# Kernel tuning notes

Hardware: AMD Instinct MI355X
Metric: run time of the kernel (lower is better)

The kernel has to match this reference:

```python
import jax, jax.numpy as jnp
import numpy as np

D_IN, D_HID = 64, 128

def _ff(x, w1, b1, w2, b2):
    # FeedForward: Linear -> ReLU -> Linear
    return jax.nn.relu(x @ w1 + b1) @ w2 + b2

def setup_inputs() -> dict:
    key = jax.random.key(0)
    ks = jax.random.split(key, 10)
    N, m = 8, 2048
    def lin(k, fan_in, fan_out):
        bound = 1.0 / np.sqrt(fan_in)
        return jax.random.uniform(k, (fan_in, fan_out), jnp.float32, -bound, bound)
    return {
        "x": jax.random.normal(ks[0], (N, m, D_IN), jnp.float32),
        "edge": jax.random.uniform(ks[1], (N, m, m), jnp.float32),
        # f: dim_in -> dim_hid//2 -> dim_hid
        "f_w1": lin(ks[2], D_IN, D_HID // 2),
        "f_b1": jnp.zeros((D_HID // 2,), jnp.float32),
        "f_w2": lin(ks[3], D_HID // 2, D_HID),
        "f_b2": jnp.zeros((D_HID,), jnp.float32),
        # g: 2*dim_in -> dim_hid -> dim_hid
        "g_w1": lin(ks[4], 2 * D_IN, D_HID),
        "g_b1": jnp.zeros((D_HID,), jnp.float32),
        "g_w2": lin(ks[5], D_HID, D_HID),
        "g_b2": jnp.zeros((D_HID,), jnp.float32),
    }

def reference(x, edge, f_w1, f_b1, f_w2, f_b2, g_w1, g_b1, g_w2, g_b2):
    # self dynamics: f(x) -> [N, m, D_HID]
    self_dyn = _ff(x, f_w1, f_b1, f_w2, f_b2)
    # Original builds interaction[n,i,j] = cat(x[n,i], x[n,i]) (receiver is
    # transposed twice), so g is constant along j. Compute g once per sender node.
    gx = _ff(jnp.concatenate([x, x], axis=-1), g_w1, g_b1, g_w2, g_b2)  # [N, m, H]
    # interaction.sum over sender dim i with edge weights: out[n,j] = sum_i edge[n,i,j]*gx[n,i]
    inter = jnp.einsum('nij,nih->njh', edge, gx)
    return self_dyn + inter
```

## Files before the change

kernel.cpp:

```cpp
#include <hip/hip_runtime.h>


typedef __attribute__((ext_vector_type(8))) short bf16x8;
typedef __attribute__((ext_vector_type(8))) unsigned short u16x8;
typedef __attribute__((ext_vector_type(4))) unsigned short u16x4;
typedef __attribute__((ext_vector_type(4))) float f32x4;
typedef __attribute__((ext_vector_type(8))) float f32x8;

static __device__ __forceinline__ unsigned short f2bf(float f) {
  union { float f; unsigned int i; } c; c.f = f;
  return (unsigned short)((c.i + 0x7fffu + ((c.i >> 16) & 1u)) >> 16);
}

__global__ __launch_bounds__(256) void k_gx(
    const float* __restrict__ x,
    const float* __restrict__ gw1,
    const float* __restrict__ gb1,
    const float* __restrict__ gw2,
    const float* __restrict__ gb2,
    unsigned short* __restrict__ gxT)
{
  __shared__ short xs[64 * 64];
  __shared__ short w1T[128 * 64];
  __shared__ short w2T[128 * 128];
  __shared__ short h2s[64 * 128];

  const int t = threadIdx.x;
  const int R0 = blockIdx.x * 64;

  for (int idx = t; idx < 64 * 128; idx += 256) {
    int k = idx >> 7, n = idx & 127;
    float v = gw1[idx] + gw1[64 * 128 + idx];
    w1T[(n << 6) + (((k >> 3) ^ (n & 7)) << 3) + (k & 7)] = (short)f2bf(v);
  }
  for (int idx = t; idx < 128 * 128; idx += 256) {
    int k = idx >> 7, n = idx & 127;
    w2T[(n << 7) + (((k >> 3) ^ (n & 7)) << 3) + (k & 7)] = (short)f2bf(gw2[idx]);
  }
  for (int s = t; s < 64 * 16; s += 256) {
    int row = s >> 4, c4 = s & 15;
    f32x4 v = *(const f32x4*)(x + (size_t)(R0 + row) * 64 + c4 * 4);
    u16x4 pk;
#pragma unroll
    for (int r = 0; r < 4; ++r) pk[r] = f2bf(v[r]);
    *(u16x4*)(xs + (row << 6) + (((c4 >> 1) ^ (row & 7)) << 3) + ((c4 & 1) << 2)) = pk;
  }
  __syncthreads();

  const int w = t >> 6, l = t & 63;
  const int lr = l & 15, q = l >> 4;
  const int mrow = w * 16 + lr;

  bf16x8 a[2];
#pragma unroll
  for (int ks = 0; ks < 2; ++ks) {
    int c = ks * 4 + q;
    a[ks] = *(const bf16x8*)(xs + (mrow << 6) + ((c ^ (mrow & 7)) << 3));
  }

  f32x4 acc;
#pragma unroll
  for (int nf = 0; nf < 8; ++nf) {
    acc = (f32x4){0.f, 0.f, 0.f, 0.f};
#pragma unroll
    for (int ks = 0; ks < 2; ++ks) {
      int c = ks * 4 + q;
      int nr = nf * 16 + lr;
      bf16x8 b = *(const bf16x8*)(w1T + (nr << 6) + ((c ^ (nr & 7)) << 3));
      acc = __builtin_amdgcn_mfma_f32_16x16x32_bf16(a[ks], b, acc, 0, 0, 0);
    }
    float bias = gb1[nf * 16 + lr];
#pragma unroll
    for (int r = 0; r < 4; ++r) {
      float v = acc[r] + bias;
      v = v > 0.f ? v : 0.f;
      int row = w * 16 + q * 4 + r, n = nf * 16 + lr;
      h2s[(row << 7) + (((n >> 3) ^ (row & 7)) << 3) + (n & 7)] = (short)f2bf(v);
    }
  }
  __syncthreads();

  bf16x8 a2[4];
#pragma unroll
  for (int ks = 0; ks < 4; ++ks) {
    int c = ks * 4 + q;
    a2[ks] = *(const bf16x8*)(h2s + (mrow << 7) + ((c ^ (mrow & 7)) << 3));
  }
  const int batch = R0 >> 11;
  const int ib = R0 & 2047;
#pragma unroll
  for (int nf = 0; nf < 8; ++nf) {
    acc = (f32x4){0.f, 0.f, 0.f, 0.f};
#pragma unroll
    for (int ks = 0; ks < 4; ++ks) {
      int c = ks * 4 + q;
      int nr = nf * 16 + lr;
      bf16x8 b = *(const bf16x8*)(w2T + (nr << 7) + ((c ^ (nr & 7)) << 3));
      acc = __builtin_amdgcn_mfma_f32_16x16x32_bf16(a2[ks], b, acc, 0, 0, 0);
    }
    float bias = gb2[nf * 16 + lr];
    u16x4 pk;
#pragma unroll
    for (int r = 0; r < 4; ++r) pk[r] = f2bf(acc[r] + bias);
    *(u16x4*)(gxT + (size_t)(batch * 128 + nf * 16 + lr) * 2048 + ib + w * 16 + q * 4) = pk;
  }
}

__device__ __forceinline__ void load_tiles(const float* ep, const unsigned short* gp,
                                           f32x8& er, u16x8 gr[4])
{
  er = *(const f32x8*)ep;
#pragma unroll
  for (int qq = 0; qq < 4; ++qq)
    gr[qq] = *(const u16x8*)(gp + (size_t)qq * 32 * 2048);
}

__global__ __launch_bounds__(256) void k_main(
    const float* __restrict__ edge,
    const unsigned short* __restrict__ gxT,
    const float* __restrict__ x,
    const float* __restrict__ fw1,
    const float* __restrict__ fb1,
    const float* __restrict__ fw2,
    const float* __restrict__ fb2,
    float* __restrict__ out)
{
  __shared__ short eT[32 * 72];
  __shared__ short bT[128 * 64];
  __shared__ short xs[32 * 64];
  __shared__ short w1T[64 * 64];
  __shared__ short h1s[32 * 64];

  const int t = threadIdx.x;
  const int batch = blockIdx.x & 7;
  const int j0 = (blockIdx.x >> 3) * 32;

  const int w = t >> 6, l = t & 63;
  const int wm = w & 1, wn = w >> 1;
  const int lr = l & 15, q = l >> 4;

  const int e_ii = t >> 2;
  const int e_cj = t & 3;
  const int g_hh = t >> 3;
  const int g_ci = t & 7;

  const float* ep = edge + (size_t)batch * 2048 * 2048 + (size_t)e_ii * 2048 + j0 + e_cj * 8;
  const unsigned short* gp = gxT + (size_t)batch * 128 * 2048 + (size_t)g_hh * 2048 + g_ci * 8;

  f32x4 acc[4];
#pragma unroll
  for (int nf = 0; nf < 4; ++nf) acc[nf] = (f32x4){0.f, 0.f, 0.f, 0.f};

  f32x8 er;
  u16x8 gr[4];
  load_tiles(ep, gp, er, gr);

  for (int kk = 0; kk < 32; ++kk) {
    __syncthreads();
#pragma unroll
    for (int u = 0; u < 8; ++u)
      eT[(e_cj * 8 + u) * 72 + (((e_ii >> 3) ^ e_cj) << 3) + (e_ii & 7)] = (short)f2bf(er[u]);
#pragma unroll
    for (int qq = 0; qq < 4; ++qq) {
      int r = qq * 32 + g_hh;
      *(u16x8*)(bT + (r << 6) + ((g_ci ^ (r & 7)) << 3)) = gr[qq];
    }
    __syncthreads();
    if (kk < 31) {
      ep += 64 * 2048; gp += 64;
      load_tiles(ep, gp, er, gr);
    }

#pragma unroll
    for (int ks = 0; ks < 2; ++ks) {
      const int c = ks * 4 + q;
      const int jj = wm * 16 + lr;
      bf16x8 a = *(const bf16x8*)(eT + jj * 72 + ((c ^ (jj >> 3)) << 3));
      bf16x8 b[4];
#pragma unroll
      for (int nf = 0; nf < 4; ++nf) {
        int h = wn * 64 + nf * 16 + lr;
        b[nf] = *(const bf16x8*)(bT + (h << 6) + ((c ^ (h & 7)) << 3));
      }
#pragma unroll
      for (int nf = 0; nf < 4; ++nf)
        acc[nf] = __builtin_amdgcn_mfma_f32_16x16x32_bf16(a, b[nf], acc[nf], 0, 0, 0);
    }
  }

  __syncthreads();
  for (int idx = t; idx < 64 * 64; idx += 256) {
    int k = idx >> 6, n = idx & 63;
    w1T[(n << 6) + (((k >> 3) ^ (n & 7)) << 3) + (k & 7)] = (short)f2bf(fw1[idx]);
  }
  for (int idx = t; idx < 64 * 128; idx += 256) {
    int k = idx >> 7, n = idx & 127;
    bT[(n << 6) + (((k >> 3) ^ (n & 7)) << 3) + (k & 7)] = (short)f2bf(fw2[idx]);
  }
  for (int s = t; s < 32 * 16; s += 256) {
    int row = s >> 4, c4 = s & 15;
    f32x4 v = *(const f32x4*)(x + (size_t)(batch * 2048 + j0 + row) * 64 + c4 * 4);
    u16x4 pk;
#pragma unroll
    for (int r = 0; r < 4; ++r) pk[r] = f2bf(v[r]);
    *(u16x4*)(xs + (row << 6) + (((c4 >> 1) ^ (row & 7)) << 3) + ((c4 & 1) << 2)) = pk;
  }
  __syncthreads();

  const int mrow = wm * 16 + lr;
  if (wn == 0) {
    bf16x8 a1[2];
#pragma unroll
    for (int ks = 0; ks < 2; ++ks) {
      int c = ks * 4 + q;
      a1[ks] = *(const bf16x8*)(xs + (mrow << 6) + ((c ^ (mrow & 7)) << 3));
    }
#pragma unroll
    for (int nf = 0; nf < 4; ++nf) {
      f32x4 h = (f32x4){0.f, 0.f, 0.f, 0.f};
#pragma unroll
      for (int ks = 0; ks < 2; ++ks) {
        int c = ks * 4 + q;
        int nr = nf * 16 + lr;
        bf16x8 b = *(const bf16x8*)(w1T + (nr << 6) + ((c ^ (nr & 7)) << 3));
        h = __builtin_amdgcn_mfma_f32_16x16x32_bf16(a1[ks], b, h, 0, 0, 0);
      }
      float bias = fb1[nf * 16 + lr];
#pragma unroll
      for (int r = 0; r < 4; ++r) {
        float v = h[r] + bias;
        v = v > 0.f ? v : 0.f;
        int row = wm * 16 + q * 4 + r, n = nf * 16 + lr;
        h1s[(row << 6) + (((n >> 3) ^ (row & 7)) << 3) + (n & 7)] = (short)f2bf(v);
      }
    }
  }
  __syncthreads();

  bf16x8 a2[2];
#pragma unroll
  for (int ks = 0; ks < 2; ++ks) {
    int c = ks * 4 + q;
    a2[ks] = *(const bf16x8*)(h1s + (mrow << 6) + ((c ^ (mrow & 7)) << 3));
  }
#pragma unroll
  for (int nf = 0; nf < 4; ++nf) {
    int h = wn * 64 + nf * 16 + lr;
#pragma unroll
    for (int ks = 0; ks < 2; ++ks) {
      int c = ks * 4 + q;
      bf16x8 b = *(const bf16x8*)(bT + (h << 6) + ((c ^ (h & 7)) << 3));
      acc[nf] = __builtin_amdgcn_mfma_f32_16x16x32_bf16(a2[ks], b, acc[nf], 0, 0, 0);
    }
    float bias = fb2[h];
#pragma unroll
    for (int r = 0; r < 4; ++r) {
      size_t o = ((size_t)batch * 2048 + j0 + wm * 16 + q * 4 + r) * 128 + h;
      out[o] = acc[nf][r] + bias;
    }
  }
}

extern "C" void kernel_launch(void* const* d_in, const int* in_sizes, int n_in,
                              void* d_out, int out_size, void* d_ws, size_t ws_size,
                              hipStream_t stream) {
  const float* x    = (const float*)d_in[0];
  const float* edge = (const float*)d_in[1];
  const float* fw1  = (const float*)d_in[2];
  const float* fb1  = (const float*)d_in[3];
  const float* fw2  = (const float*)d_in[4];
  const float* fb2  = (const float*)d_in[5];
  const float* gw1  = (const float*)d_in[6];
  const float* gb1  = (const float*)d_in[7];
  const float* gw2  = (const float*)d_in[8];
  const float* gb2  = (const float*)d_in[9];
  float* out = (float*)d_out;

  unsigned short* gxT = (unsigned short*)d_ws;

  hipLaunchKernelGGL(k_gx, dim3(256), dim3(256), 0, stream, x, gw1, gb1, gw2, gb2, gxT);
  hipLaunchKernelGGL(k_main, dim3(512), dim3(256), 0, stream, edge, gxT, x,
                     fw1, fb1, fw2, fb2, out);
}
```

Baseline: 239.6 us.

## Double-buffer edge and gx tiles in LDS with one barrier per iteration

Adds ping-pong LDS buffers for the transposed edge tile and the gx tile, so the next tile is written to shared memory while MFMAs consume the current one. This removes one of the two __syncthreads per k-step and issues global loads two tiles ahead. The edge load mapping also changes: each thread now loads two float4 rows and packs pairs of bf16 values into 32-bit LDS stores instead of eight 16-bit scalar stores. LDS use grows by about 20KB per block, which may reduce occupancy.

New measurement: 242.4 us. No clear change (+1.2%).

```diff
diff --git a/kernel.cpp b/kernel.cpp
--- a/kernel.cpp
+++ b/kernel.cpp
@@ -5,7 +5,6 @@
 typedef __attribute__((ext_vector_type(8))) unsigned short u16x8;
 typedef __attribute__((ext_vector_type(4))) unsigned short u16x4;
 typedef __attribute__((ext_vector_type(4))) float f32x4;
-typedef __attribute__((ext_vector_type(8))) float f32x8;
 
 static __device__ __forceinline__ unsigned short f2bf(float f) {
   union { float f; unsigned int i; } c; c.f = f;
@@ -106,15 +105,6 @@
   }
 }
 
-__device__ __forceinline__ void load_tiles(const float* ep, const unsigned short* gp,
-                                           f32x8& er, u16x8 gr[4])
-{
-  er = *(const f32x8*)ep;
-#pragma unroll
-  for (int qq = 0; qq < 4; ++qq)
-    gr[qq] = *(const u16x8*)(gp + (size_t)qq * 32 * 2048);
-}
-
 __global__ __launch_bounds__(256) void k_main(
     const float* __restrict__ edge,
     const unsigned short* __restrict__ gxT,
@@ -125,8 +115,8 @@
     const float* __restrict__ fb2,
     float* __restrict__ out)
 {
-  __shared__ short eT[32 * 72];
-  __shared__ short bT[128 * 64];
+  __shared__ short eT[2][32 * 72];
+  __shared__ short bT[2][128 * 64];
   __shared__ short xs[32 * 64];
   __shared__ short w1T[64 * 64];
   __shared__ short h1s[32 * 64];
@@ -139,63 +129,93 @@
   const int wm = w & 1, wn = w >> 1;
   const int lr = l & 15, q = l >> 4;
 
-  const int e_ii = t >> 2;
-  const int e_cj = t & 3;
+  const int p  = t >> 3;
+  const int cq = t & 7;
   const int g_hh = t >> 3;
   const int g_ci = t & 7;
 
-  const float* ep = edge + (size_t)batch * 2048 * 2048 + (size_t)e_ii * 2048 + j0 + e_cj * 8;
+  const float* ep = edge + (size_t)batch * 2048 * 2048 + (size_t)(2 * p) * 2048 + j0 + 4 * cq;
   const unsigned short* gp = gxT + (size_t)batch * 128 * 2048 + (size_t)g_hh * 2048 + g_ci * 8;
 
+  f32x4 er0, er1;
+  u16x8 gr[4];
+
+  er0 = *(const f32x4*)ep;
+  er1 = *(const f32x4*)(ep + 2048);
+#pragma unroll
+  for (int qq = 0; qq < 4; ++qq) gr[qq] = *(const u16x8*)(gp + (size_t)qq * 32 * 2048);
+
   f32x4 acc[4];
 #pragma unroll
   for (int nf = 0; nf < 4; ++nf) acc[nf] = (f32x4){0.f, 0.f, 0.f, 0.f};
 
-  f32x8 er;
-  u16x8 gr[4];
-  load_tiles(ep, gp, er, gr);
+#pragma unroll
+  for (int u = 0; u < 4; ++u) {
+    int j = 4 * cq + u;
+    unsigned int pk = (unsigned int)f2bf(er0[u]) | ((unsigned int)f2bf(er1[u]) << 16);
+    *(unsigned int*)(&eT[0][j * 72 + (((p >> 2) ^ (j >> 3)) << 3) + ((p & 3) << 1)]) = pk;
+  }
+#pragma unroll
+  for (int qq = 0; qq < 4; ++qq) {
+    int r = qq * 32 + g_hh;
+    *(u16x8*)(&bT[0][(r << 6) + ((g_ci ^ (r & 7)) << 3)]) = gr[qq];
+  }
+  ep += 64 * 2048; gp += 64;
+  er0 = *(const f32x4*)ep;
+  er1 = *(const f32x4*)(ep + 2048);
+#pragma unroll
+  for (int qq = 0; qq < 4; ++qq) gr[qq] = *(const u16x8*)(gp + (size_t)qq * 32 * 2048);
+  __syncthreads();
 
   for (int kk = 0; kk < 32; ++kk) {
-    __syncthreads();
-#pragma unroll
-    for (int u = 0; u < 8; ++u)
-      eT[(e_cj * 8 + u) * 72 + (((e_ii >> 3) ^ e_cj) << 3) + (e_ii & 7)] = (short)f2bf(er[u]);
-#pragma unroll
-    for (int qq = 0; qq < 4; ++qq) {
-      int r = qq * 32 + g_hh;
-      *(u16x8*)(bT + (r << 6) + ((g_ci ^ (r & 7)) << 3)) = gr[qq];
-    }
-    __syncthreads();
+    const int cur = kk & 1;
     if (kk < 31) {
-      ep += 64 * 2048; gp += 64;
-      load_tiles(ep, gp, er, gr);
+      const int nxt = cur ^ 1;
+#pragma unroll
+      for (int u = 0; u < 4; ++u) {
+        int j = 4 * cq + u;
+        unsigned int pk = (unsigned int)f2bf(er0[u]) | ((unsigned int)f2bf(er1[u]) << 16);
+        *(unsigned int*)(&eT[nxt][j * 72 + (((p >> 2) ^ (j >> 3)) << 3) + ((p & 3) << 1)]) = pk;
+      }
+#pragma unroll
+      for (int qq = 0; qq < 4; ++qq) {
+        int r = qq * 32 + g_hh;
+        *(u16x8*)(&bT[nxt][(r << 6) + ((g_ci ^ (r & 7)) << 3)]) = gr[qq];
+      }
+      if (kk < 30) {
+        ep += 64 * 2048; gp += 64;
+        er0 = *(const f32x4*)ep;
+        er1 = *(const f32x4*)(ep + 2048);
+#pragma unroll
+        for (int qq = 0; qq < 4; ++qq) gr[qq] = *(const u16x8*)(gp + (size_t)qq * 32 * 2048);
+      }
     }
 
 #pragma unroll
     for (int ks = 0; ks < 2; ++ks) {
       const int c = ks * 4 + q;
       const int jj = wm * 16 + lr;
-      bf16x8 a = *(const bf16x8*)(eT + jj * 72 + ((c ^ (jj >> 3)) << 3));
+      bf16x8 a = *(const bf16x8*)(&eT[cur][jj * 72 + ((c ^ (jj >> 3)) << 3)]);
       bf16x8 b[4];
 #pragma unroll
       for (int nf = 0; nf < 4; ++nf) {
         int h = wn * 64 + nf * 16 + lr;
-        b[nf] = *(const bf16x8*)(bT + (h << 6) + ((c ^ (h & 7)) << 3));
+        b[nf] = *(const bf16x8*)(&bT[cur][(h << 6) + ((c ^ (h & 7)) << 3)]);
       }
 #pragma unroll
       for (int nf = 0; nf < 4; ++nf)
         acc[nf] = __builtin_amdgcn_mfma_f32_16x16x32_bf16(a, b[nf], acc[nf], 0, 0, 0);
     }
-  }
-
-  __syncthreads();
+    __syncthreads();
+  }
+
   for (int idx = t; idx < 64 * 64; idx += 256) {
     int k = idx >> 6, n = idx & 63;
     w1T[(n << 6) + (((k >> 3) ^ (n & 7)) << 3) + (k & 7)] = (short)f2bf(fw1[idx]);
   }
   for (int idx = t; idx < 64 * 128; idx += 256) {
     int k = idx >> 7, n = idx & 127;
-    bT[(n << 6) + (((k >> 3) ^ (n & 7)) << 3) + (k & 7)] = (short)f2bf(fw2[idx]);
+    bT[0][(n << 6) + (((k >> 3) ^ (n & 7)) << 3) + (k & 7)] = (short)f2bf(fw2[idx]);
   }
   for (int s = t; s < 32 * 16; s += 256) {
     int row = s >> 4, c4 = s & 15;
@@ -249,7 +269,7 @@
 #pragma unroll
     for (int ks = 0; ks < 2; ++ks) {
       int c = ks * 4 + q;
-      bf16x8 b = *(const bf16x8*)(bT + (h << 6) + ((c ^ (h & 7)) << 3));
+      bf16x8 b = *(const bf16x8*)(&bT[0][(h << 6) + ((c ^ (h & 7)) << 3)]);
       acc[nf] = __builtin_amdgcn_mfma_f32_16x16x32_bf16(a2[ks], b, acc[nf], 0, 0, 0);
     }
     float bias = fb2[h];
```
